# Performance work log

Measured on AMD Instinct MI355X. Metric: run time of the kernel, lower is better.

The kernel has to match this reference:

```python
import jax, jax.numpy as jnp
import numpy as np

B, C, H, W = 256, 256, 14, 14
CH = C // 2  # 128
N = H * W    # 196
EPS = 1e-5


def setup_inputs() -> dict:
    key = jax.random.key(0)
    ks = jax.random.split(key, 8)
    return {
        "x": jax.random.normal(ks[0], (B, C, H, W), jnp.float32),
        "y": jax.random.normal(ks[1], (B, C, H, W), jnp.float32),
        "Wq": jax.random.normal(ks[2], (CH, C), jnp.float32) * 0.05,
        "Wk": jax.random.normal(ks[3], (CH, C), jnp.float32) * 0.05,
        "Wv": jax.random.normal(ks[4], (CH, C), jnp.float32) * 0.05,
        "Wz": jax.random.normal(ks[5], (C, CH), jnp.float32) * 0.05,
        "bn_weight": jnp.ones((C,), jnp.float32),
        "bn_bias": jnp.zeros((C,), jnp.float32),
        "bn_mean": jax.random.normal(ks[6], (C,), jnp.float32) * 0.1,
        "bn_var": jax.random.uniform(ks[7], (C,), jnp.float32, 0.5, 1.5),
    }


def reference(x, y, Wq, Wk, Wv, Wz, bn_weight, bn_bias, bn_mean, bn_var):
    b = x.shape[0]
    xf = x.reshape(b, C, N)  # [B, C, N]
    yf = y.reshape(b, C, N)
    # 1x1 convs == channel matmuls
    Q = jnp.einsum('oc,bcn->bon', Wq, xf)  # [B, CH, N]
    K = jnp.einsum('oc,bcn->bon', Wk, yf)
    V = jnp.einsum('oc,bcn->bon', Wv, yf)
    # M = Q^T K  -> [B, N, N]
    M = jnp.einsum('bcq,bck->bqk', Q, K)
    # Softmax2d over a singleton channel dim (faithful to original: yields ones)
    M = jax.nn.softmax(M[:, None, :, :], axis=1)[:, 0]
    Z = jnp.einsum('bcn,bnm->bcm', V, M)  # [B, CH, N]
    Z = jnp.einsum('oc,bcn->bon', Wz, Z)  # [B, C, N]
    Z = Z.reshape(b, C, H, W)
    # BatchNorm2d (inference form with running stats)
    inv = jax.lax.rsqrt(bn_var + EPS)
    Z = (Z - bn_mean[:, None, None]) * (inv * bn_weight)[:, None, None] + bn_bias[:, None, None]
    return x + Z
```

## Files before the change

kernel.cpp:

```cpp
#include <hip/hip_runtime.h>

#define B_   256
#define C_   256
#define CH_  128
#define N_   196
#define NF4  49
#define NROW4 12544
#define EPS  1e-5f

__global__ __launch_bounds__(256) void k_wzvt(const float* __restrict__ Wz,
                                              const float* __restrict__ Wv,
                                              const float* __restrict__ bnw,
                                              const float* __restrict__ bnv,
                                              float* __restrict__ WzvTs) {
    __shared__ float sWv[CH_];
    int c = blockIdx.x;
    int o = threadIdx.x;
    if (o < CH_) sWv[o] = Wv[o * C_ + c];
    __syncthreads();
    const float4* wzrow = (const float4*)(Wz + o * CH_);
    float acc = 0.f;
    #pragma unroll
    for (int k4 = 0; k4 < CH_ / 4; k4++) {
        float4 w = wzrow[k4];
        acc += w.x * sWv[4 * k4 + 0];
        acc += w.y * sWv[4 * k4 + 1];
        acc += w.z * sWv[4 * k4 + 2];
        acc += w.w * sWv[4 * k4 + 3];
    }
    float alpha = bnw[o] * rsqrtf(bnv[o] + EPS);
    WzvTs[c * C_ + o] = acc * alpha;
}

__global__ __launch_bounds__(1024, 4) void k_main(const float* __restrict__ x,
                                                  const float* __restrict__ y,
                                                  const float* __restrict__ WzvTs,
                                                  const float* __restrict__ bnw,
                                                  const float* __restrict__ bnb,
                                                  const float* __restrict__ bnm,
                                                  const float* __restrict__ bnv,
                                                  float* __restrict__ out) {
    __shared__ float sY[C_];
    __shared__ float sPart[4][C_];
    __shared__ float sZ[C_];

    int b    = blockIdx.x;
    int tid  = threadIdx.x;
    int w    = tid >> 6;
    int lane = tid & 63;

    const float4* yb = (const float4*)y + (size_t)b * NROW4;
    #pragma unroll
    for (int i = 0; i < 16; i += 4) {
        float s[4];
        #pragma unroll
        for (int j = 0; j < 4; j++) {
            int r = (w << 4) + i + j;
            float4 v = make_float4(0.f, 0.f, 0.f, 0.f);
            if (lane < NF4) v = yb[r * NF4 + lane];
            s[j] = (v.x + v.y) + (v.z + v.w);
        }
        #pragma unroll
        for (int off = 32; off > 0; off >>= 1) {
            #pragma unroll
            for (int j = 0; j < 4; j++) s[j] += __shfl_down(s[j], off, 64);
        }
        if (lane == 0) {
            #pragma unroll
            for (int j = 0; j < 4; j++) sY[(w << 4) + i + j] = s[j];
        }
    }
    __syncthreads();

    {
        int o   = tid & (C_ - 1);
        int seg = tid >> 8;
        int c0  = seg * 64;
        float acc = 0.f;
        #pragma unroll 8
        for (int c = 0; c < 64; c++)
            acc += sY[c0 + c] * WzvTs[(c0 + c) * C_ + o];
        sPart[seg][o] = acc;
    }
    __syncthreads();
    if (tid < C_) {
        float z = sPart[0][tid] + sPart[1][tid] + sPart[2][tid] + sPart[3][tid];
        float alpha = bnw[tid] * rsqrtf(bnv[tid] + EPS);
        sZ[tid] = z + bnb[tid] - bnm[tid] * alpha;
    }
    __syncthreads();

    const float4* xb = (const float4*)x   + (size_t)b * NROW4;
    float4*       ob = (float4*)out       + (size_t)b * NROW4;
    #pragma unroll
    for (int k = 0; k < 12; k++) {
        int idx = tid + (k << 10);
        int r = idx / NF4;
        float z = sZ[r];
        float4 v = xb[idx];
        v.x += z; v.y += z; v.z += z; v.w += z;
        ob[idx] = v;
    }
    {
        int idx = tid + (12 << 10);
        if (idx < NROW4) {
            int r = idx / NF4;
            float z = sZ[r];
            float4 v = xb[idx];
            v.x += z; v.y += z; v.z += z; v.w += z;
            ob[idx] = v;
        }
    }
}

extern "C" void kernel_launch(void* const* d_in, const int* in_sizes, int n_in,
                              void* d_out, int out_size, void* d_ws, size_t ws_size,
                              hipStream_t stream) {
    const float* x   = (const float*)d_in[0];
    const float* y   = (const float*)d_in[1];
    const float* Wv  = (const float*)d_in[4];
    const float* Wz  = (const float*)d_in[5];
    const float* bnw = (const float*)d_in[6];
    const float* bnb = (const float*)d_in[7];
    const float* bnm = (const float*)d_in[8];
    const float* bnv = (const float*)d_in[9];
    float* out = (float*)d_out;

    float* WzvTs = (float*)d_ws;

    k_wzvt<<<C_, 256, 0, stream>>>(Wz, Wv, bnw, bnv, WzvTs);
    k_main<<<B_, 1024, 0, stream>>>(x, y, WzvTs, bnw, bnb, bnm, bnv, out);
}
```

Baseline: 167.3 us.

## Split per-batch Z computation from broadcast-add into a separate wide elementwise kernel

Result: slower. 172.0 us (+2.8%).

```diff
diff --git a/kernel.cpp b/kernel.cpp
--- a/kernel.cpp
+++ b/kernel.cpp
@@ -1,48 +1,25 @@
 #include <hip/hip_runtime.h>
 
-#define B_   256
-#define C_   256
-#define CH_  128
-#define N_   196
-#define NF4  49
+#define B_    256
+#define C_    256
+#define CH_   128
+#define N_    196
+#define NF4   49
 #define NROW4 12544
-#define EPS  1e-5f
+#define EPS   1e-5f
 
-__global__ __launch_bounds__(256) void k_wzvt(const float* __restrict__ Wz,
-                                              const float* __restrict__ Wv,
-                                              const float* __restrict__ bnw,
-                                              const float* __restrict__ bnv,
-                                              float* __restrict__ WzvTs) {
-    __shared__ float sWv[CH_];
-    int c = blockIdx.x;
-    int o = threadIdx.x;
-    if (o < CH_) sWv[o] = Wv[o * C_ + c];
-    __syncthreads();
-    const float4* wzrow = (const float4*)(Wz + o * CH_);
-    float acc = 0.f;
-    #pragma unroll
-    for (int k4 = 0; k4 < CH_ / 4; k4++) {
-        float4 w = wzrow[k4];
-        acc += w.x * sWv[4 * k4 + 0];
-        acc += w.y * sWv[4 * k4 + 1];
-        acc += w.z * sWv[4 * k4 + 2];
-        acc += w.w * sWv[4 * k4 + 3];
-    }
-    float alpha = bnw[o] * rsqrtf(bnv[o] + EPS);
-    WzvTs[c * C_ + o] = acc * alpha;
-}
+typedef float f32x4 __attribute__((ext_vector_type(4)));
 
-__global__ __launch_bounds__(1024, 4) void k_main(const float* __restrict__ x,
-                                                  const float* __restrict__ y,
-                                                  const float* __restrict__ WzvTs,
-                                                  const float* __restrict__ bnw,
-                                                  const float* __restrict__ bnb,
-                                                  const float* __restrict__ bnm,
-                                                  const float* __restrict__ bnv,
-                                                  float* __restrict__ out) {
+__global__ __launch_bounds__(1024) void k_zs(const float* __restrict__ y,
+                                             const float* __restrict__ Wv,
+                                             const float* __restrict__ Wz,
+                                             const float* __restrict__ bnw,
+                                             const float* __restrict__ bnb,
+                                             const float* __restrict__ bnm,
+                                             const float* __restrict__ bnv,
+                                             float* __restrict__ Zs) {
     __shared__ float sY[C_];
-    __shared__ float sPart[4][C_];
-    __shared__ float sZ[C_];
+    __shared__ float sT[CH_];
 
     int b    = blockIdx.x;
     int tid  = threadIdx.x;
@@ -72,45 +49,41 @@
     }
     __syncthreads();
 
-    {
-        int o   = tid & (C_ - 1);
-        int seg = tid >> 8;
-        int c0  = seg * 64;
-        float acc = 0.f;
-        #pragma unroll 8
-        for (int c = 0; c < 64; c++)
-            acc += sY[c0 + c] * WzvTs[(c0 + c) * C_ + o];
-        sPart[seg][o] = acc;
-    }
-    __syncthreads();
-    if (tid < C_) {
-        float z = sPart[0][tid] + sPart[1][tid] + sPart[2][tid] + sPart[3][tid];
-        float alpha = bnw[tid] * rsqrtf(bnv[tid] + EPS);
-        sZ[tid] = z + bnb[tid] - bnm[tid] * alpha;
+    #pragma unroll
+    for (int j = 0; j < 8; j++) {
+        int k = (w << 3) + j;
+        float4 wv = ((const float4*)(Wv + k * C_))[lane];
+        float s = wv.x * sY[4 * lane + 0] + wv.y * sY[4 * lane + 1]
+                + wv.z * sY[4 * lane + 2] + wv.w * sY[4 * lane + 3];
+        #pragma unroll
+        for (int off = 32; off > 0; off >>= 1) s += __shfl_down(s, off, 64);
+        if (lane == 0) sT[k] = s;
     }
     __syncthreads();
 
-    const float4* xb = (const float4*)x   + (size_t)b * NROW4;
-    float4*       ob = (float4*)out       + (size_t)b * NROW4;
     #pragma unroll
-    for (int k = 0; k < 12; k++) {
-        int idx = tid + (k << 10);
-        int r = idx / NF4;
-        float z = sZ[r];
-        float4 v = xb[idx];
-        v.x += z; v.y += z; v.z += z; v.w += z;
-        ob[idx] = v;
-    }
-    {
-        int idx = tid + (12 << 10);
-        if (idx < NROW4) {
-            int r = idx / NF4;
-            float z = sZ[r];
-            float4 v = xb[idx];
-            v.x += z; v.y += z; v.z += z; v.w += z;
-            ob[idx] = v;
+    for (int j = 0; j < 16; j++) {
+        int o = (w << 4) + j;
+        float2 wz = ((const float2*)(Wz + o * CH_))[lane];
+        float s = wz.x * sT[2 * lane + 0] + wz.y * sT[2 * lane + 1];
+        #pragma unroll
+        for (int off = 32; off > 0; off >>= 1) s += __shfl_down(s, off, 64);
+        if (lane == 0) {
+            float alpha = bnw[o] * rsqrtf(bnv[o] + EPS);
+            Zs[b * C_ + o] = s * alpha + bnb[o] - bnm[o] * alpha;
         }
     }
+}
+
+__global__ __launch_bounds__(256) void k_out(const float* __restrict__ x,
+                                             const float* __restrict__ Zs,
+                                             float* __restrict__ out) {
+    int idx = blockIdx.x * blockDim.x + threadIdx.x;
+    int row = idx / NF4;
+    float z = Zs[row];
+    f32x4 v = ((const f32x4*)x)[idx];
+    v.x += z; v.y += z; v.z += z; v.w += z;
+    __builtin_nontemporal_store(v, (f32x4*)out + idx);
 }
 
 extern "C" void kernel_launch(void* const* d_in, const int* in_sizes, int n_in,
@@ -126,8 +99,8 @@
     const float* bnv = (const float*)d_in[9];
     float* out = (float*)d_out;
 
-    float* WzvTs = (float*)d_ws;
+    float* Zs = (float*)d_ws;
 
-    k_wzvt<<<C_, 256, 0, stream>>>(Wz, Wv, bnw, bnv, WzvTs);
-    k_main<<<B_, 1024, 0, stream>>>(x, y, WzvTs, bnw, bnb, bnm, bnv, out);
+    k_zs<<<B_, 1024, 0, stream>>>(y, Wv, Wz, bnw, bnb, bnm, bnv, Zs);
+    k_out<<<(B_ * C_ * NF4) / 256, 256, 0, stream>>>(x, Zs, out);
 }
```
